# Kernel optimization log

Hardware: AMD Instinct MI355X
Metric: run time of the kernel (lower is better)

The kernel has to match this reference:

```python
import jax, jax.numpy as jnp
import numpy as np

N_CLUSTERS = 8
N_DIMS = 4
N_POINTS = 2_000_000


def setup_inputs() -> dict:
    key = jax.random.key(0)
    k1, k2, k3, k4 = jax.random.split(key, 4)
    return {
        "X": jax.random.normal(k1, (N_POINTS, N_DIMS), dtype=jnp.float32),
        "means": jax.random.normal(k2, (N_CLUSTERS, N_DIMS), dtype=jnp.float32),
        "chols": jax.random.normal(k3, (N_CLUSTERS, N_DIMS, N_DIMS), dtype=jnp.float32),
        "weights": jax.random.normal(k4, (N_CLUSTERS,), dtype=jnp.float32),
        "it": 0,
    }


def reference(X, means, chols, weights, it):
    N, D = X.shape
    K = means.shape[0]
    # sigmas[k] = tril(L_k) @ tril(L_k)^T + I  (cholesky_comp)
    L = jnp.tril(chols)                                   # [K,D,D]
    sigmas = L @ jnp.swapaxes(L, -1, -2) + jnp.eye(D, dtype=X.dtype)
    S_inv = jnp.linalg.inv(sigmas)                        # [K,D,D]
    dets = jnp.linalg.det(sigmas)                         # [K]
    two_pi_D = (2.0 * jnp.pi) ** D
    # per-cluster Gaussian densities over all points: dens[k,n]
    diff = X[None, :, :] - means[:, None, :]              # [K,N,D]
    mahal = jnp.einsum('knd,kde,kne->kn', diff, S_inv, diff)  # [K,N]
    dens = jnp.exp(-0.5 * mahal) / jnp.sqrt(two_pi_D * dets)[:, None]
    # pairwise softmax weights over all K^2 (i,j) products w_i*w_j
    wij = weights[:, None] * weights[None, :]             # [K,K]
    W = jax.nn.softmax(wij.reshape(-1)).reshape(K, K)
    # squared-mixture normaliser: z = sum_ij W_ij * N(mu_i; mu_j, S_i+S_j)
    Ssum = sigmas[:, None] + sigmas[None, :]              # [K,K,D,D]
    det_sum = jnp.linalg.det(Ssum)                        # [K,K]
    mdiff = means[:, None, :] - means[None, :, :]         # [K,K,D]
    md = jnp.einsum('ijd,ijde,ije->ij', mdiff, jnp.linalg.inv(Ssum), mdiff)
    norm_term = jnp.exp(-0.5 * md) / jnp.sqrt(two_pi_D * det_sum)
    z = jnp.sum(W * norm_term)
    # numerator: sum_ij W_ij dens_i dens_j  (factored to avoid [K^2,N])
    num = jnp.einsum('in,jn,ij->n', dens, dens, W)        # [N]
    pdf = num / z
    # forward: -(logsumexp over points of log pdf) / N
    out = -(jax.scipy.special.logsumexp(jnp.log(pdf)) / N)
    return out
```

## Files before the change

### kernel.cpp

```cpp
#include <hip/hip_runtime.h>
#include <math.h>


struct WsLayout {
  double tot[512];
  double logz;
  unsigned int ctr;
  unsigned int pad_;
  float par[160];
};

__device__ inline void chol4(const double S[4][4], double G[4][4]) {
  #pragma unroll
  for (int i = 0; i < 4; ++i) {
    #pragma unroll
    for (int j = 0; j < 4; ++j) {
      if (j > i) { G[i][j] = 0.0; continue; }
      double s = S[i][j];
      #pragma unroll
      for (int m = 0; m < 4; ++m) if (m < j) s -= G[i][m] * G[j][m];
      if (i == j) G[i][j] = sqrt(s);
      else        G[i][j] = s / G[j][j];
    }
  }
}

__global__ void prep_kernel(const float* __restrict__ means,
                            const float* __restrict__ chols,
                            const float* __restrict__ weights,
                            WsLayout* ws) {
  __shared__ double sig[8][4][4];
  const double LOG2E = 1.4426950408889634074;
  const double LN2PI = 1.8378770664093454836;
  const int t = threadIdx.x;

  if (t < 8) {
    const int k = t;
    double L[4][4], S[4][4];
    #pragma unroll
    for (int i = 0; i < 4; ++i)
      #pragma unroll
      for (int j = 0; j < 4; ++j)
        L[i][j] = (j <= i) ? (double)chols[k * 16 + i * 4 + j] : 0.0;
    #pragma unroll
    for (int i = 0; i < 4; ++i)
      #pragma unroll
      for (int j = 0; j < 4; ++j) {
        double s = (i == j) ? 1.0 : 0.0;
        #pragma unroll
        for (int m = 0; m < 4; ++m) s += L[i][m] * L[j][m];
        S[i][j] = s;
        sig[k][i][j] = s;
      }
    double G[4][4];
    chol4(S, G);
    const double logdet =
        2.0 * (log(G[0][0]) + log(G[1][1]) + log(G[2][2]) + log(G[3][3]));
    double Gi[4][4];
    #pragma unroll
    for (int j = 0; j < 4; ++j) {
      #pragma unroll
      for (int i = 0; i < 4; ++i) {
        if (i < j) { Gi[i][j] = 0.0; continue; }
        double s = (i == j) ? 1.0 : 0.0;
        #pragma unroll
        for (int m = 0; m < 4; ++m)
          if (m >= j && m < i) s -= G[i][m] * Gi[m][j];
        Gi[i][j] = s / G[i][i];
      }
    }
    const double sc = sqrt(0.5 * LOG2E);
    double mu[4];
    #pragma unroll
    for (int i = 0; i < 4; ++i) mu[i] = (double)means[k * 4 + i];
    int idx = 0;
    #pragma unroll
    for (int i = 0; i < 4; ++i) {
      double ti = 0.0;
      #pragma unroll
      for (int j = 0; j < 4; ++j) {
        const double gij = sc * Gi[i][j];
        if (j <= i) ws->par[k * 15 + (idx++)] = (float)gij;
        ti += gij * mu[j];
      }
      ws->par[k * 15 + 10 + i] = (float)(-ti);
    }
    const double logcoef = -0.5 * (4.0 * LN2PI + logdet);
    ws->par[k * 15 + 14] = (float)(LOG2E * logcoef);
  }
  __syncthreads();

  const int i = t >> 3, j = t & 7;
  const double wij = (double)weights[i] * (double)weights[j];
  double m = wij;
  #pragma unroll
  for (int o = 32; o > 0; o >>= 1) {
    double x = __shfl_xor(m, o, 64);
    m = fmax(m, x);
  }
  const double e = exp(wij - m);
  double ssum = e;
  #pragma unroll
  for (int o = 32; o > 0; o >>= 1) ssum += __shfl_xor(ssum, o, 64);
  const double Wij = e / ssum;

  if (i <= j) {
    const int u = 8 * i - (i * (i - 1)) / 2 + (j - i);
    ws->par[120 + u] = (float)(Wij * ((i == j) ? 1.0 : 2.0));
  }

  double SS[4][4];
  #pragma unroll
  for (int a = 0; a < 4; ++a)
    #pragma unroll
    for (int b = 0; b < 4; ++b) SS[a][b] = sig[i][a][b] + sig[j][a][b];
  double G2[4][4];
  chol4(SS, G2);
  const double logdetS =
      2.0 * (log(G2[0][0]) + log(G2[1][1]) + log(G2[2][2]) + log(G2[3][3]));
  double bvec[4], y[4];
  #pragma unroll
  for (int a = 0; a < 4; ++a)
    bvec[a] = (double)means[i * 4 + a] - (double)means[j * 4 + a];
  #pragma unroll
  for (int a = 0; a < 4; ++a) {
    double s = bvec[a];
    #pragma unroll
    for (int mm = 0; mm < 4; ++mm) if (mm < a) s -= G2[a][mm] * y[mm];
    y[a] = s / G2[a][a];
  }
  const double md = y[0]*y[0] + y[1]*y[1] + y[2]*y[2] + y[3]*y[3];
  double zterm = Wij * exp(-0.5 * md - 0.5 * (4.0 * LN2PI + logdetS));
  #pragma unroll
  for (int o = 32; o > 0; o >>= 1) zterm += __shfl_xor(zterm, o, 64);
  if (t == 0) { ws->logz = log(zterm); ws->ctr = 0u; }

  for (int u = t; u < 512; u += 64) ws->tot[u] = 0.0;
}

__device__ inline float point_s(const float4 v, const float g[8][10],
                                const float tn[8][4], const float cc[8],
                                const float W2[36]) {
  float d[8];
  #pragma unroll
  for (int k = 0; k < 8; ++k) {
    const float y0 = fmaf(g[k][0], v.x, tn[k][0]);
    const float y1 = fmaf(g[k][2], v.y, fmaf(g[k][1], v.x, tn[k][1]));
    const float y2 =
        fmaf(g[k][5], v.z, fmaf(g[k][4], v.y, fmaf(g[k][3], v.x, tn[k][2])));
    const float y3 = fmaf(
        g[k][9], v.w,
        fmaf(g[k][8], v.z, fmaf(g[k][7], v.y, fmaf(g[k][6], v.x, tn[k][3]))));
    float a = cc[k];
    a = fmaf(y0, -y0, a);
    a = fmaf(y1, -y1, a);
    a = fmaf(y2, -y2, a);
    a = fmaf(y3, -y3, a);
    d[k] = __builtin_amdgcn_exp2f(a);
  }
  float s = 0.0f;
  int u = 0;
  #pragma unroll
  for (int i = 0; i < 8; ++i) {
    float tt = W2[u++] * d[i];
    #pragma unroll
    for (int j = i + 1; j < 8; ++j) tt = fmaf(W2[u++], d[j], tt);
    s = fmaf(d[i], tt, s);
  }
  return s;
}

__global__ void point_kernel(const float4* __restrict__ X,
                             const WsLayout* __restrict__ wsc,
                             double* __restrict__ tot, unsigned int* ctr,
                             float* __restrict__ out, int n) {
  const int lane = threadIdx.x & 63;
  const int wid = threadIdx.x >> 6;
  const float* par = wsc->par;

  float g[8][10], tn[8][4], cc[8], W2[36];
  #pragma unroll
  for (int k = 0; k < 8; ++k) {
    #pragma unroll
    for (int u = 0; u < 10; ++u) g[k][u] = par[k * 15 + u];
    #pragma unroll
    for (int u = 0; u < 4; ++u) tn[k][u] = par[k * 15 + 10 + u];
    cc[k] = par[k * 15 + 14];
  }
  #pragma unroll
  for (int u = 0; u < 36; ++u) W2[u] = par[120 + u];

  #pragma unroll
  for (int k = 5; k < 8; ++k) {
    #pragma unroll
    for (int u = 0; u < 10; ++u) asm volatile("" : "+v"(g[k][u]));
    #pragma unroll
    for (int u = 0; u < 4; ++u) asm volatile("" : "+v"(tn[k][u]));
    asm volatile("" : "+v"(cc[k]));
  }
  #pragma unroll
  for (int u = 0; u < 36; ++u) asm volatile("" : "+v"(W2[u]));

  const int S = gridDim.x * blockDim.x;
  float sacc = 0.0f;
  int i = blockIdx.x * blockDim.x + threadIdx.x;
  for (; i + S < n; i += 2 * S) {
    const float4 va = X[i];
    const float4 vb = X[i + S];
    sacc += point_s(va, g, tn, cc, W2);
    sacc += point_s(vb, g, tn, cc, W2);
  }
  for (; i < n; i += S) sacc += point_s(X[i], g, tn, cc, W2);

  double bs = (double)sacc;
  #pragma unroll
  for (int o = 32; o > 0; o >>= 1) bs += __shfl_xor(bs, o, 64);
  __shared__ double lred[4];
  if (lane == 0) lred[wid] = bs;
  __syncthreads();
  if (threadIdx.x == 0) {
    const double v = lred[0] + lred[1] + lred[2] + lred[3];
    unsafeAtomicAdd(&tot[(blockIdx.x & 63) * 8], v);
  }
  __syncthreads();

  __shared__ int amLast;
  if (threadIdx.x == 0) {
    __threadfence();
    const unsigned int old = atomicAdd(ctr, 1u);
    amLast = (old == gridDim.x - 1u);
    __threadfence();
  }
  __syncthreads();
  if (amLast && threadIdx.x < 64) {
    double val = unsafeAtomicAdd(&tot[threadIdx.x * 8], 0.0);
    #pragma unroll
    for (int o = 32; o > 0; o >>= 1) val += __shfl_xor(val, o, 64);
    if (threadIdx.x == 0)
      out[0] = (float)(-(log(val) - wsc->logz) / (double)n);
  }
}

extern "C" void kernel_launch(void* const* d_in, const int* in_sizes, int n_in,
                              void* d_out, int out_size, void* d_ws, size_t ws_size,
                              hipStream_t stream) {
  const float* X       = (const float*)d_in[0];
  const float* means   = (const float*)d_in[1];
  const float* chols   = (const float*)d_in[2];
  const float* weights = (const float*)d_in[3];
  const int npoints = in_sizes[0] / 4;

  WsLayout* ws = (WsLayout*)d_ws;
  prep_kernel<<<1, 64, 0, stream>>>(means, chols, weights, ws);
  point_kernel<<<1024, 256, 0, stream>>>((const float4*)X, ws, ws->tot,
                                         &ws->ctr, (float*)d_out, npoints);
}
```

Measured before the change: 131.2 us.

## Fold per-cluster normalisation constants into pair weights and unroll point loop by four

Each cluster's log normaliser is moved out of the per-point exponent and folded into the pairwise weight matrix as exp2(c_i + c_j). This removes one add per cluster per point and cuts eight uniform parameters. The point loop now loads four points per iteration instead of two, launch bounds force one block per CU, and all parameters are pinned in VGPRs instead of only some. The risks are extra register pressure and float precision, since the tiny folded weight scales could underflow or lose accuracy in fp32.

```diff
diff --git a/kernel.cpp b/kernel.cpp
--- a/kernel.cpp
+++ b/kernel.cpp
@@ -7,7 +7,7 @@
   double logz;
   unsigned int ctr;
   unsigned int pad_;
-  float par[160];
+  float par[148];
 };
 
 __device__ inline void chol4(const double S[4][4], double G[4][4]) {
@@ -30,6 +30,7 @@
                             const float* __restrict__ weights,
                             WsLayout* ws) {
   __shared__ double sig[8][4][4];
+  __shared__ double ccs[8];
   const double LOG2E = 1.4426950408889634074;
   const double LN2PI = 1.8378770664093454836;
   const int t = threadIdx.x;
@@ -80,13 +81,12 @@
       #pragma unroll
       for (int j = 0; j < 4; ++j) {
         const double gij = sc * Gi[i][j];
-        if (j <= i) ws->par[k * 15 + (idx++)] = (float)gij;
+        if (j <= i) ws->par[k * 14 + (idx++)] = (float)gij;
         ti += gij * mu[j];
       }
-      ws->par[k * 15 + 10 + i] = (float)(-ti);
+      ws->par[k * 14 + 10 + i] = (float)(-ti);
     }
-    const double logcoef = -0.5 * (4.0 * LN2PI + logdet);
-    ws->par[k * 15 + 14] = (float)(LOG2E * logcoef);
+    ccs[k] = LOG2E * (-0.5 * (4.0 * LN2PI + logdet));
   }
   __syncthreads();
 
@@ -106,7 +106,8 @@
 
   if (i <= j) {
     const int u = 8 * i - (i * (i - 1)) / 2 + (j - i);
-    ws->par[120 + u] = (float)(Wij * ((i == j) ? 1.0 : 2.0));
+    const double scale = exp2(ccs[i] + ccs[j]) * ((i == j) ? 1.0 : 2.0);
+    ws->par[112 + u] = (float)(Wij * scale);
   }
 
   double SS[4][4];
@@ -139,8 +140,7 @@
 }
 
 __device__ inline float point_s(const float4 v, const float g[8][10],
-                                const float tn[8][4], const float cc[8],
-                                const float W2[36]) {
+                                const float tn[8][4], const float W2[36]) {
   float d[8];
   #pragma unroll
   for (int k = 0; k < 8; ++k) {
@@ -151,12 +151,11 @@
     const float y3 = fmaf(
         g[k][9], v.w,
         fmaf(g[k][8], v.z, fmaf(g[k][7], v.y, fmaf(g[k][6], v.x, tn[k][3]))));
-    float a = cc[k];
-    a = fmaf(y0, -y0, a);
-    a = fmaf(y1, -y1, a);
-    a = fmaf(y2, -y2, a);
-    a = fmaf(y3, -y3, a);
-    d[k] = __builtin_amdgcn_exp2f(a);
+    float q = y0 * y0;
+    q = fmaf(y1, y1, q);
+    q = fmaf(y2, y2, q);
+    q = fmaf(y3, y3, q);
+    d[k] = __builtin_amdgcn_exp2f(-q);
   }
   float s = 0.0f;
   int u = 0;
@@ -170,47 +169,49 @@
   return s;
 }
 
-__global__ void point_kernel(const float4* __restrict__ X,
-                             const WsLayout* __restrict__ wsc,
-                             double* __restrict__ tot, unsigned int* ctr,
-                             float* __restrict__ out, int n) {
+__global__ __launch_bounds__(256, 1) void point_kernel(
+    const float4* __restrict__ X, const WsLayout* __restrict__ wsc,
+    double* __restrict__ tot, unsigned int* ctr, float* __restrict__ out,
+    int n) {
   const int lane = threadIdx.x & 63;
   const int wid = threadIdx.x >> 6;
   const float* par = wsc->par;
 
-  float g[8][10], tn[8][4], cc[8], W2[36];
+  float g[8][10], tn[8][4], W2[36];
   #pragma unroll
   for (int k = 0; k < 8; ++k) {
     #pragma unroll
-    for (int u = 0; u < 10; ++u) g[k][u] = par[k * 15 + u];
-    #pragma unroll
-    for (int u = 0; u < 4; ++u) tn[k][u] = par[k * 15 + 10 + u];
-    cc[k] = par[k * 15 + 14];
-  }
-  #pragma unroll
-  for (int u = 0; u < 36; ++u) W2[u] = par[120 + u];
-
-  #pragma unroll
-  for (int k = 5; k < 8; ++k) {
-    #pragma unroll
-    for (int u = 0; u < 10; ++u) asm volatile("" : "+v"(g[k][u]));
-    #pragma unroll
-    for (int u = 0; u < 4; ++u) asm volatile("" : "+v"(tn[k][u]));
-    asm volatile("" : "+v"(cc[k]));
-  }
-  #pragma unroll
-  for (int u = 0; u < 36; ++u) asm volatile("" : "+v"(W2[u]));
+    for (int u = 0; u < 10; ++u) g[k][u] = par[k * 14 + u];
+    #pragma unroll
+    for (int u = 0; u < 4; ++u) tn[k][u] = par[k * 14 + 10 + u];
+  }
+  #pragma unroll
+  for (int u = 0; u < 36; ++u) W2[u] = par[112 + u];
+
+  #pragma unroll
+  for (int k = 0; k < 8; ++k) {
+    #pragma unroll
+    for (int u = 0; u < 10; ++u) asm("" : "+v"(g[k][u]));
+    #pragma unroll
+    for (int u = 0; u < 4; ++u) asm("" : "+v"(tn[k][u]));
+  }
+  #pragma unroll
+  for (int u = 0; u < 36; ++u) asm("" : "+v"(W2[u]));
 
   const int S = gridDim.x * blockDim.x;
   float sacc = 0.0f;
   int i = blockIdx.x * blockDim.x + threadIdx.x;
-  for (; i + S < n; i += 2 * S) {
-    const float4 va = X[i];
-    const float4 vb = X[i + S];
-    sacc += point_s(va, g, tn, cc, W2);
-    sacc += point_s(vb, g, tn, cc, W2);
-  }
-  for (; i < n; i += S) sacc += point_s(X[i], g, tn, cc, W2);
+  for (; i + 3 * S < n; i += 4 * S) {
+    const float4 v0 = X[i];
+    const float4 v1 = X[i + S];
+    const float4 v2 = X[i + 2 * S];
+    const float4 v3 = X[i + 3 * S];
+    sacc += point_s(v0, g, tn, W2);
+    sacc += point_s(v1, g, tn, W2);
+    sacc += point_s(v2, g, tn, W2);
+    sacc += point_s(v3, g, tn, W2);
+  }
+  for (; i < n; i += S) sacc += point_s(X[i], g, tn, W2);
 
   double bs = (double)sacc;
   #pragma unroll
```

Result: slower. 136.0 us (+3.7%).
